# Performance work log

Measured on AMD Instinct MI355X. Metric: run time of the kernel, lower is better.

Reference implementation:

```python
import jax, jax.numpy as jnp
import numpy as np

B, S, D, H = 2, 2048, 1024, 16
HD = D // H  # head_dim = 64


def setup_inputs() -> dict:
    key = jax.random.key(0)
    ks = jax.random.split(key, 6)
    scale = D ** -0.5
    x = jax.random.normal(ks[0], (B, S, D), dtype=jnp.float32)
    wq = jax.random.normal(ks[1], (D, D), dtype=jnp.float32) * scale
    wk = jax.random.normal(ks[2], (D, D), dtype=jnp.float32) * scale
    wv = jax.random.normal(ks[3], (D, D), dtype=jnp.float32) * scale
    wo = jax.random.normal(ks[4], (D, D), dtype=jnp.float32) * scale
    # RoPE frequencies: theta_i = 10000^(-2i/HD), angles[t, i] = t * theta_i
    inv_freq = 1.0 / (10000.0 ** (np.arange(0, HD, 2, dtype=np.float32) / HD))
    t = np.arange(S, dtype=np.float32)
    angles = np.outer(t, inv_freq)  # [S, HD//2]
    freqs_cos = jnp.asarray(np.cos(angles), dtype=jnp.float32)
    freqs_sin = jnp.asarray(np.sin(angles), dtype=jnp.float32)
    # additive causal mask [1,1,S,S]
    neg = jnp.float32(-1e9)
    mask = jnp.triu(jnp.full((S, S), neg, dtype=jnp.float32), k=1)[None, None]
    return {"x": x, "wq": wq, "wk": wk, "wv": wv, "wo": wo,
            "freqs_cos": freqs_cos, "freqs_sin": freqs_sin,
            "mask": mask, "start_pos": 0}


def _apply_rope(q, freqs_cos, freqs_sin):
    # q: [B, S, H, HD] -> pairs (even, odd) rotated by angle per position
    b, s, h, hd = q.shape
    q2 = q.reshape(b, s, h, hd // 2, 2)
    qr, qi = q2[..., 0], q2[..., 1]
    c = freqs_cos[None, :, None, :]  # [1, S, 1, HD//2]
    sn = freqs_sin[None, :, None, :]
    out_r = qr * c - qi * sn
    out_i = qr * sn + qi * c
    return jnp.stack([out_r, out_i], axis=-1).reshape(b, s, h, hd)


def reference(x, wq, wk, wv, wo, freqs_cos, freqs_sin, mask, start_pos):
    b, s, _ = x.shape
    xq = (x @ wq).reshape(b, s, H, HD)
    xk = (x @ wk).reshape(b, s, H, HD)
    xv = (x @ wv).reshape(b, s, H, HD)
    xq = _apply_rope(xq, freqs_cos, freqs_sin)
    xk = _apply_rope(xk, freqs_cos, freqs_sin)
    # [B, H, S, HD]
    q = xq.transpose(0, 2, 1, 3)
    k = xk.transpose(0, 2, 1, 3)
    v = xv.transpose(0, 2, 1, 3)
    scores = jnp.einsum('bhqd,bhkd->bhqk', q, k) / jnp.sqrt(jnp.float32(HD))
    scores = scores + mask
    probs = jax.nn.softmax(scores.astype(jnp.float32), axis=-1).astype(q.dtype)
    out = jnp.einsum('bhqk,bhkd->bhqd', probs, v)
    out = out.transpose(0, 2, 1, 3).reshape(b, s, H * HD)
    return out @ wo
```

## Files before the change

kernel.cpp:

```cpp
#include <hip/hip_runtime.h>

typedef unsigned short u16;
typedef __bf16 bf16x8 __attribute__((ext_vector_type(8)));
typedef float f32x4 __attribute__((ext_vector_type(4)));

#define DD 1024
#define SS 2048
#define HH 16
#define HDIM 64

__device__ __forceinline__ u16 f2bf(float f) {
  union { float f; unsigned u; } x; x.f = f;
  unsigned r = x.u + 0x7FFFu + ((x.u >> 16) & 1u);
  return (u16)(r >> 16);
}

__device__ __forceinline__ u16 f2bf_s(float f) {
  unsigned r;
  asm("v_cvt_pk_bf16_f32 %0, %1, %2" : "=v"(r) : "v"(f), "v"(0.f));
  return (u16)r;
}

__device__ __forceinline__ void gload_lds16(const u16* g, u16* l) {
  __builtin_amdgcn_global_load_lds((const __attribute__((address_space(1))) void*)g,
                                   (__attribute__((address_space(3))) void*)l, 16, 0, 0);
}

__global__ __launch_bounds__(256) void prep(const float* __restrict__ x,
                                            const float* __restrict__ w0, const float* __restrict__ w1,
                                            const float* __restrict__ w2, const float* __restrict__ w3,
                                            u16* __restrict__ xb, u16* __restrict__ wT) {
  __shared__ float t[32][33];
  const int id = blockIdx.x;
  const int tid = threadIdx.x;
  if (id < 4096) {
    int i = (id * 256 + tid) * 4;
    float4 v = *(const float4*)(x + i);
    xb[i + 0] = f2bf(v.x);
    xb[i + 1] = f2bf(v.y);
    xb[i + 2] = f2bf(v.z);
    xb[i + 3] = f2bf(v.w);
    return;
  }
  const int tt = id - 4096;
  const int z = tt >> 10;
  const int xy = tt & 1023;
  const int j0 = (xy & 31) * 32;
  const int i0 = (xy >> 5) * 32;
  const float* w = (z == 0) ? w0 : (z == 1) ? w1 : (z == 2) ? w2 : w3;
  u16* o = wT + (size_t)z * DD * DD;
  const int tx = tid & 31, ty = tid >> 5;
#pragma unroll
  for (int r = ty; r < 32; r += 8)
    t[r][tx] = w[(size_t)(i0 + r) * DD + j0 + tx];
  __syncthreads();
#pragma unroll
  for (int r = ty; r < 32; r += 8)
    o[(size_t)(j0 + r) * DD + i0 + tx] = f2bf(t[tx][r]);
}

__global__ __launch_bounds__(512, 2) void gemm_qkv(const u16* __restrict__ xb, const u16* __restrict__ wT,
                                                   const float* __restrict__ fc, const float* __restrict__ fs,
                                                   u16* __restrict__ Qr, u16* __restrict__ Kr, u16* __restrict__ Vt) {
  __shared__ u16 As[3][128 * 64];
  __shared__ u16 Bs[3][192 * 64];
  const int tid = threadIdx.x;
  const int lane = tid & 63, wid = tid >> 6;
  const int wm = wid >> 2, wn = wid & 3;
  const int lr = lane & 15, lg = lane >> 4;
  const int m0 = blockIdx.x * 128, n0 = blockIdx.y * 192;

  f32x4 acc[4][3];
#pragma unroll
  for (int i = 0; i < 4; ++i)
#pragma unroll
    for (int j = 0; j < 3; ++j) acc[i][j] = (f32x4){0.f, 0.f, 0.f, 0.f};

  auto stage = [&](int buf, int k0) {
#pragma unroll
    for (int i = 0; i < 2; ++i) {
      int c = tid + i * 512;
      int row = c >> 3, j = (c & 7) ^ (row & 7);
      gload_lds16(xb + (size_t)(m0 + row) * DD + k0 + j * 8, &As[buf][c * 8]);
    }
#pragma unroll
    for (int i = 0; i < 3; ++i) {
      int c = tid + i * 512;
      int row = c >> 3, j = (c & 7) ^ (row & 7);
      gload_lds16(wT + (size_t)(n0 + row) * DD + k0 + j * 8, &Bs[buf][c * 8]);
    }
  };

  stage(0, 0);
  int cur = 0;
  for (int kt = 0; kt < 16; ++kt) {
    if (kt < 15) {
      int nxt = (cur == 2) ? 0 : cur + 1;
      stage(nxt, (kt + 1) * 64);
      asm volatile("s_waitcnt vmcnt(5)" ::: "memory");
    } else {
      asm volatile("s_waitcnt vmcnt(0)" ::: "memory");
    }
    __builtin_amdgcn_s_barrier();
    __builtin_amdgcn_sched_barrier(0);
#pragma unroll
    for (int ks = 0; ks < 2; ++ks) {
      bf16x8 af[4], bfr[3];
#pragma unroll
      for (int mi = 0; mi < 4; ++mi) {
        int row = wm * 64 + mi * 16 + lr;
        int ch = (ks * 4 + lg) ^ (row & 7);
        af[mi] = *(const bf16x8*)(&As[cur][row * 64 + ch * 8]);
      }
#pragma unroll
      for (int ni = 0; ni < 3; ++ni) {
        int row = wn * 48 + ni * 16 + lr;
        int ch = (ks * 4 + lg) ^ (row & 7);
        bfr[ni] = *(const bf16x8*)(&Bs[cur][row * 64 + ch * 8]);
      }
      __builtin_amdgcn_s_setprio(1);
#pragma unroll
      for (int mi = 0; mi < 4; ++mi)
#pragma unroll
        for (int ni = 0; ni < 3; ++ni)
          acc[mi][ni] = __builtin_amdgcn_mfma_f32_16x16x32_bf16(af[mi], bfr[ni], acc[mi][ni], 0, 0, 0);
      __builtin_amdgcn_s_setprio(0);
    }
    cur = (cur == 2) ? 0 : cur + 1;
  }

#pragma unroll
  for (int mi = 0; mi < 4; ++mi)
#pragma unroll
    for (int ni = 0; ni < 3; ++ni) {
      const int nb = n0 + wn * 48 + ni * 16;
      const int z = nb >> 10;
      const int nn = (nb & 1023) + lr;
      const int h = nn >> 6, hd = nn & 63;
#pragma unroll
      for (int j = 0; j < 4; ++j) {
        int m = m0 + wm * 64 + mi * 16 + lg * 4 + j;
        float v = acc[mi][ni][j];
        int b = m >> 11, s = m & 2047;
        if (z == 2) {
          Vt[((size_t)(b * HH + h) * HDIM + hd) * SS + s] = f2bf(v);
        } else {
          float pv = __shfl_xor(v, 1);
          int fi = s * 32 + (hd >> 1);
          float c = fc[fi], sn = fs[fi];
          float o = ((hd & 1) == 0) ? (v * c - pv * sn) : (pv * sn + v * c);
          u16* dst = (z == 0) ? Qr : Kr;
          dst[((size_t)(b * HH + h) * SS + s) * HDIM + hd] = f2bf(o);
        }
      }
    }
}

__device__ __forceinline__ void stage_tile(const u16* __restrict__ Kh, const u16* __restrict__ Vh,
                                           int i2, u16* Kbuf, u16* Vbuf, int tid) {
#pragma unroll
  for (int k = 0; k < 2; ++k) {
    const int c = tid + k * 512;
    const int tt = c >> 9, cl = c & 511;
    const int row = cl >> 3, j = (cl & 7) ^ (row & 7);
    gload_lds16(Kh + (size_t)(i2 * 128 + tt * 64 + row) * HDIM + j * 8, Kbuf + c * 8);
    gload_lds16(Vh + (size_t)row * SS + i2 * 128 + tt * 64 + j * 8, Vbuf + c * 8);
  }
}

__device__ __forceinline__ void attn_pass(int qt, int bh, const u16* __restrict__ Qh,
                                          const u16* __restrict__ Kh, const u16* __restrict__ Vh,
                                          u16* __restrict__ Ob, u16* KbR, u16* VbR, u16* Pw,
                                          int gid, int wq) {
  const int tid = threadIdx.x;
  const int lane = tid & 63;
  const int lr = lane & 15, lg = lane >> 4;
  const int q0 = qt * 64 + wq * 16;

  bf16x8 aq[2];
#pragma unroll
  for (int ks = 0; ks < 2; ++ks)
    aq[ks] = *(const bf16x8*)(Qh + (q0 + lr) * HDIM + ks * 32 + lg * 8);

  bf16x8 ones;
  {
    union { u16 u[8]; bf16x8 v; } ou;
#pragma unroll
    for (int i = 0; i < 8; ++i) ou.u[i] = 0x3F80;
    ones = ou.v;
  }

  f32x4 o[4];
#pragma unroll
  for (int d = 0; d < 4; ++d) o[d] = (f32x4){0.f, 0.f, 0.f, 0.f};
  f32x4 ls = (f32x4){0.f, 0.f, 0.f, 0.f};

  const int n2 = (qt + 2) >> 1;

  __syncthreads();
  stage_tile(Kh, Vh, 0, KbR, VbR, tid);

  for (int i = 0; i < n2; ++i) {
    const int cur = i & 1;
    __syncthreads();
    if (i + 1 < n2) stage_tile(Kh, Vh, i + 1, KbR + (cur ^ 1) * 8192, VbR + (cur ^ 1) * 8192, tid);

    const int t = 2 * i + gid;
    const u16* Kt = KbR + cur * 8192 + gid * 4096;
    const u16* Vtl = VbR + cur * 8192 + gid * 4096;

    f32x4 sc[4];
#pragma unroll
    for (int kb = 0; kb < 4; ++kb) sc[kb] = (f32x4){0.f, 0.f, 0.f, 0.f};
    __builtin_amdgcn_s_setprio(1);
#pragma unroll
    for (int ks = 0; ks < 2; ++ks)
#pragma unroll
      for (int kb = 0; kb < 4; ++kb) {
        int row = kb * 16 + lr;
        int ch = (ks * 4 + lg) ^ (row & 7);
        bf16x8 bk = *(const bf16x8*)(Kt + row * 64 + ch * 8);
        sc[kb] = __builtin_amdgcn_mfma_f32_16x16x32_bf16(aq[ks], bk, sc[kb], 0, 0, 0);
      }
    __builtin_amdgcn_s_setprio(0);

    if (t >= qt) {
#pragma unroll
      for (int kb = 0; kb < 4; ++kb)
#pragma unroll
        for (int j = 0; j < 4; ++j) {
          int q = q0 + lg * 4 + j;
          int kk = t * 64 + kb * 16 + lr;
          float e = __expf(sc[kb][j] * 0.125f);
          sc[kb][j] = (kk > q) ? 0.f : e;
        }
    } else {
#pragma unroll
      for (int kb = 0; kb < 4; ++kb)
#pragma unroll
        for (int j = 0; j < 4; ++j)
          sc[kb][j] = __expf(sc[kb][j] * 0.125f);
    }

#pragma unroll
    for (int kb = 0; kb < 4; ++kb)
#pragma unroll
      for (int j = 0; j < 4; ++j) {
        int rr = lg * 4 + j;
        int ccol = kb * 16 + lr;
        int ch = (ccol >> 3) ^ (rr & 7);
        Pw[rr * 64 + ch * 8 + (ccol & 7)] = f2bf_s(sc[kb][j]);
      }
#pragma unroll
    for (int ks = 0; ks < 2; ++ks) {
      int chp = (ks * 4 + lg) ^ (lr & 7);
      bf16x8 ap = *(const bf16x8*)(Pw + lr * 64 + chp * 8);
      __builtin_amdgcn_s_setprio(1);
      ls = __builtin_amdgcn_mfma_f32_16x16x32_bf16(ap, ones, ls, 0, 0, 0);
#pragma unroll
      for (int d = 0; d < 4; ++d) {
        int row = d * 16 + lr;
        int ch = (ks * 4 + lg) ^ (row & 7);
        bf16x8 bv = *(const bf16x8*)(Vtl + row * 64 + ch * 8);
        o[d] = __builtin_amdgcn_mfma_f32_16x16x32_bf16(ap, bv, o[d], 0, 0, 0);
      }
      __builtin_amdgcn_s_setprio(0);
    }
  }

  __syncthreads();
  float* mo = (float*)KbR;
  float* ml = (float*)VbR;
  if (gid == 1) {
#pragma unroll
    for (int d = 0; d < 4; ++d)
#pragma unroll
      for (int j = 0; j < 4; ++j)
        mo[(wq * 16 + lg * 4 + j) * 64 + d * 16 + lr] = o[d][j];
    if (lr == 0) {
#pragma unroll
      for (int j = 0; j < 4; ++j) ml[wq * 16 + lg * 4 + j] = ls[j];
    }
  }
  __syncthreads();
  if (gid == 0) {
    const int b = bh >> 4, h = bh & 15;
#pragma unroll
    for (int j = 0; j < 4; ++j) ls[j] += ml[wq * 16 + lg * 4 + j];
#pragma unroll
    for (int d = 0; d < 4; ++d)
#pragma unroll
      for (int j = 0; j < 4; ++j) {
        float val = o[d][j] + mo[(wq * 16 + lg * 4 + j) * 64 + d * 16 + lr];
        int s = q0 + lg * 4 + j;
        int col = h * HDIM + d * 16 + lr;
        Ob[((size_t)b * SS + s) * DD + col] = f2bf(val / ls[j]);
      }
  }
}

__global__ __launch_bounds__(512, 4) void attn(const u16* __restrict__ Qr, const u16* __restrict__ Kr,
                                               const u16* __restrict__ Vt, u16* __restrict__ Ob) {
  __shared__ u16 Kb[2][2][64 * 64];
  __shared__ u16 Vb[2][2][64 * 64];
  __shared__ u16 Ps[8][16 * 64];
  const int id = blockIdx.x;
  const int xcd = id & 7;
  const int r = id >> 3;
  const int pair = r & 15;
  const int bh = xcd * 4 + (r >> 4);
  const u16* Qh = Qr + (size_t)bh * SS * HDIM;
  const u16* Kh = Kr + (size_t)bh * SS * HDIM;
  const u16* Vh = Vt + (size_t)bh * HDIM * SS;
  const int wid = threadIdx.x >> 6;
  const int gid = wid >> 2, wq = wid & 3;
  u16* Pw = &Ps[wid][0];
  attn_pass(pair, bh, Qh, Kh, Vh, Ob, &Kb[0][0][0], &Vb[0][0][0], Pw, gid, wq);
  attn_pass(31 - pair, bh, Qh, Kh, Vh, Ob, &Kb[0][0][0], &Vb[0][0][0], Pw, gid, wq);
}

__global__ __launch_bounds__(512, 2) void gemm_wo(const u16* __restrict__ Ab, const u16* __restrict__ woT,
                                                  float* __restrict__ out) {
  __shared__ u16 As[3][128 * 64];
  __shared__ u16 Bs[3][128 * 64];
  const int tid = threadIdx.x;
  const int lane = tid & 63, wid = tid >> 6;
  const int wm = wid >> 1, wn = wid & 1;
  const int lr = lane & 15, lg = lane >> 4;
  const int m0 = blockIdx.x * 128, n0 = blockIdx.y * 128;

  f32x4 acc[2][4];
#pragma unroll
  for (int i = 0; i < 2; ++i)
#pragma unroll
    for (int j = 0; j < 4; ++j) acc[i][j] = (f32x4){0.f, 0.f, 0.f, 0.f};

  auto stage = [&](int buf, int k0) {
#pragma unroll
    for (int i = 0; i < 2; ++i) {
      int c = tid + i * 512;
      int row = c >> 3, j = (c & 7) ^ (row & 7);
      gload_lds16(Ab + (size_t)(m0 + row) * DD + k0 + j * 8, &As[buf][c * 8]);
      gload_lds16(woT + (size_t)(n0 + row) * DD + k0 + j * 8, &Bs[buf][c * 8]);
    }
  };

  stage(0, 0);
  int cur = 0;
  for (int kt = 0; kt < 16; ++kt) {
    if (kt < 15) {
      int nxt = (cur == 2) ? 0 : cur + 1;
      stage(nxt, (kt + 1) * 64);
      asm volatile("s_waitcnt vmcnt(4)" ::: "memory");
    } else {
      asm volatile("s_waitcnt vmcnt(0)" ::: "memory");
    }
    __builtin_amdgcn_s_barrier();
    __builtin_amdgcn_sched_barrier(0);
#pragma unroll
    for (int ks = 0; ks < 2; ++ks) {
      bf16x8 af[2], bfr[4];
#pragma unroll
      for (int mi = 0; mi < 2; ++mi) {
        int row = wm * 32 + mi * 16 + lr;
        int ch = (ks * 4 + lg) ^ (row & 7);
        af[mi] = *(const bf16x8*)(&As[cur][row * 64 + ch * 8]);
      }
#pragma unroll
      for (int ni = 0; ni < 4; ++ni) {
        int row = wn * 64 + ni * 16 + lr;
        int ch = (ks * 4 + lg) ^ (row & 7);
        bfr[ni] = *(const bf16x8*)(&Bs[cur][row * 64 + ch * 8]);
      }
      __builtin_amdgcn_s_setprio(1);
#pragma unroll
      for (int mi = 0; mi < 2; ++mi)
#pragma unroll
        for (int ni = 0; ni < 4; ++ni)
          acc[mi][ni] = __builtin_amdgcn_mfma_f32_16x16x32_bf16(af[mi], bfr[ni], acc[mi][ni], 0, 0, 0);
      __builtin_amdgcn_s_setprio(0);
    }
    cur = (cur == 2) ? 0 : cur + 1;
  }

#pragma unroll
  for (int mi = 0; mi < 2; ++mi)
#pragma unroll
    for (int ni = 0; ni < 4; ++ni)
#pragma unroll
      for (int j = 0; j < 4; ++j) {
        int m = m0 + wm * 32 + mi * 16 + lg * 4 + j;
        int n = n0 + wn * 64 + ni * 16 + lr;
        out[(size_t)m * DD + n] = acc[mi][ni][j];
      }
}

extern "C" void kernel_launch(void* const* d_in, const int* in_sizes, int n_in,
                              void* d_out, int out_size, void* d_ws, size_t ws_size,
                              hipStream_t stream) {
  const float* x  = (const float*)d_in[0];
  const float* wq = (const float*)d_in[1];
  const float* wk = (const float*)d_in[2];
  const float* wv = (const float*)d_in[3];
  const float* wo = (const float*)d_in[4];
  const float* fc = (const float*)d_in[5];
  const float* fs = (const float*)d_in[6];
  float* out = (float*)d_out;

  char* ws = (char*)d_ws;
  u16* xb = (u16*)(ws);
  u16* wT = (u16*)(ws + (8ull << 20));
  u16* Qr = (u16*)(ws + (16ull << 20));
  u16* Kr = (u16*)(ws + (24ull << 20));
  u16* Vt = (u16*)(ws + (32ull << 20));
  u16* Ob = (u16*)(ws + (40ull << 20));

  prep<<<8192, 256, 0, stream>>>(x, wq, wk, wv, wo, xb, wT);
  gemm_qkv<<<dim3(32, 16), 512, 0, stream>>>(xb, wT, fc, fs, Qr, Kr, Vt);
  attn<<<512, 512, 0, stream>>>(Qr, Kr, Vt, Ob);
  gemm_wo<<<dim3(32, 8), 512, 0, stream>>>(Ob, wT + 3ull * DD * DD, out);
}
```

Measured before the change: 115.9 us.

## Switch GEMMs to double buffering with explicit barriers and raise occupancy bound

The QKV and output-projection GEMMs go from triple to double LDS buffering. Each iteration now starts with a barrier that waits for outstanding LDS reads before the next tile is staged, and their launch bounds are raised to allow four blocks per CU. Halving LDS use per block is meant to let more blocks stay resident to hide latency, at the cost of the prefetch distance dropping to one stage and an extra barrier per k-step. The attention loop replaces __syncthreads with the same split waitcnt/barrier scheme, so loads for the next tile can overlap work on the current one.

```diff
diff --git a/kernel.cpp b/kernel.cpp
--- a/kernel.cpp
+++ b/kernel.cpp
@@ -8,6 +8,11 @@
 #define SS 2048
 #define HH 16
 #define HDIM 64
+
+#define VMCNT(N) asm volatile("s_waitcnt vmcnt(" #N ")" ::: "memory")
+#define LGKMCNT0 asm volatile("s_waitcnt lgkmcnt(0)" ::: "memory")
+#define MEMFENCE asm volatile("" ::: "memory")
+#define SBAR __builtin_amdgcn_s_barrier()
 
 __device__ __forceinline__ u16 f2bf(float f) {
   union { float f; unsigned u; } x; x.f = f;
@@ -59,11 +64,11 @@
     o[(size_t)(j0 + r) * DD + i0 + tx] = f2bf(t[tx][r]);
 }
 
-__global__ __launch_bounds__(512, 2) void gemm_qkv(const u16* __restrict__ xb, const u16* __restrict__ wT,
+__global__ __launch_bounds__(512, 4) void gemm_qkv(const u16* __restrict__ xb, const u16* __restrict__ wT,
                                                    const float* __restrict__ fc, const float* __restrict__ fs,
                                                    u16* __restrict__ Qr, u16* __restrict__ Kr, u16* __restrict__ Vt) {
-  __shared__ u16 As[3][128 * 64];
-  __shared__ u16 Bs[3][192 * 64];
+  __shared__ u16 As[2][128 * 64];
+  __shared__ u16 Bs[2][192 * 64];
   const int tid = threadIdx.x;
   const int lane = tid & 63, wid = tid >> 6;
   const int wm = wid >> 2, wn = wid & 3;
@@ -92,17 +97,16 @@
   };
 
   stage(0, 0);
-  int cur = 0;
   for (int kt = 0; kt < 16; ++kt) {
+    const int cur = kt & 1;
+    LGKMCNT0; SBAR;
     if (kt < 15) {
-      int nxt = (cur == 2) ? 0 : cur + 1;
-      stage(nxt, (kt + 1) * 64);
-      asm volatile("s_waitcnt vmcnt(5)" ::: "memory");
+      stage(cur ^ 1, (kt + 1) * 64);
+      VMCNT(5);
     } else {
-      asm volatile("s_waitcnt vmcnt(0)" ::: "memory");
-    }
-    __builtin_amdgcn_s_barrier();
-    __builtin_amdgcn_sched_barrier(0);
+      VMCNT(0);
+    }
+    SBAR; MEMFENCE;
 #pragma unroll
     for (int ks = 0; ks < 2; ++ks) {
       bf16x8 af[4], bfr[3];
@@ -126,7 +130,6 @@
           acc[mi][ni] = __builtin_amdgcn_mfma_f32_16x16x32_bf16(af[mi], bfr[ni], acc[mi][ni], 0, 0, 0);
       __builtin_amdgcn_s_setprio(0);
     }
-    cur = (cur == 2) ? 0 : cur + 1;
   }
 
 #pragma unroll
@@ -202,8 +205,14 @@
 
   for (int i = 0; i < n2; ++i) {
     const int cur = i & 1;
-    __syncthreads();
-    if (i + 1 < n2) stage_tile(Kh, Vh, i + 1, KbR + (cur ^ 1) * 8192, VbR + (cur ^ 1) * 8192, tid);
+    LGKMCNT0; SBAR;
+    if (i + 1 < n2) {
+      stage_tile(Kh, Vh, i + 1, KbR + (cur ^ 1) * 8192, VbR + (cur ^ 1) * 8192, tid);
+      VMCNT(4);
+    } else {
+      VMCNT(0);
+    }
+    SBAR; MEMFENCE;
 
     const int t = 2 * i + gid;
     const u16* Kt = KbR + cur * 8192 + gid * 4096;
@@ -319,10 +328,10 @@
   attn_pass(31 - pair, bh, Qh, Kh, Vh, Ob, &Kb[0][0][0], &Vb[0][0][0], Pw, gid, wq);
 }
 
-__global__ __launch_bounds__(512, 2) void gemm_wo(const u16* __restrict__ Ab, const u16* __restrict__ woT,
+__global__ __launch_bounds__(512, 4) void gemm_wo(const u16* __restrict__ Ab, const u16* __restrict__ woT,
                                                   float* __restrict__ out) {
-  __shared__ u16 As[3][128 * 64];
-  __shared__ u16 Bs[3][128 * 64];
+  __shared__ u16 As[2][128 * 64];
+  __shared__ u16 Bs[2][128 * 64];
   const int tid = threadIdx.x;
   const int lane = tid & 63, wid = tid >> 6;
   const int wm = wid >> 1, wn = wid & 1;
@@ -346,17 +355,16 @@
   };
 
   stage(0, 0);
-  int cur = 0;
   for (int kt = 0; kt < 16; ++kt) {
+    const int cur = kt & 1;
+    LGKMCNT0; SBAR;
     if (kt < 15) {
-      int nxt = (cur == 2) ? 0 : cur + 1;
-      stage(nxt, (kt + 1) * 64);
-      asm volatile("s_waitcnt vmcnt(4)" ::: "memory");
+      stage(cur ^ 1, (kt + 1) * 64);
+      VMCNT(4);
     } else {
-      asm volatile("s_waitcnt vmcnt(0)" ::: "memory");
-    }
-    __builtin_amdgcn_s_barrier();
-    __builtin_amdgcn_sched_barrier(0);
+      VMCNT(0);
+    }
+    SBAR; MEMFENCE;
 #pragma unroll
     for (int ks = 0; ks < 2; ++ks) {
       bf16x8 af[2], bfr[4];
@@ -380,7 +388,6 @@
           acc[mi][ni] = __builtin_amdgcn_mfma_f32_16x16x32_bf16(af[mi], bfr[ni], acc[mi][ni], 0, 0, 0);
       __builtin_amdgcn_s_setprio(0);
     }
-    cur = (cur == 2) ? 0 : cur + 1;
   }
 
 #pragma unroll
```

New measurement: 113.4 us. 1.02x faster.
